# Optimization experiments

Measured on AMD Instinct MI355X. Metric: run time of the kernel, lower is better.

Reference implementation:

```python
import jax, jax.numpy as jnp
import numpy as np

B, S, D = 4, 2048, 512
H, DK = 8, 64
FFN = 2048
LEFT, CHUNK, RIGHT = 512, 128, 128
EPS = 1e-5


def _emformer_mask():
    # True = disallowed. Each query attends to its own chunk, LEFT keys before
    # the chunk start, and RIGHT keys after the chunk end.
    idx = jnp.arange(S)
    cs = (idx // CHUNK) * CHUNK                      # chunk start per query
    j = idx[None, :]
    allowed = (j >= cs[:, None] - LEFT) & (j < cs[:, None] + CHUNK + RIGHT)
    return jnp.broadcast_to(~allowed, (B, 1, S, S))


def _ln(x, g, b):
    m = jnp.mean(x, axis=-1, keepdims=True)
    v = jnp.var(x, axis=-1, keepdims=True)
    return (x - m) * jax.lax.rsqrt(v + EPS) * g + b


def setup_inputs() -> dict:
    key = jax.random.key(0)
    ks = jax.random.split(key, 8)
    w = lambda k, shp: jax.random.normal(k, shp, dtype=jnp.float32) * 0.02
    return {
        "x": jax.random.normal(ks[0], (B, S, D), dtype=jnp.float32),
        "mask": _emformer_mask(),
        "ln_in_g": jnp.ones((D,), jnp.float32), "ln_in_b": jnp.zeros((D,), jnp.float32),
        "wq": w(ks[1], (D, D)), "bq": jnp.zeros((D,), jnp.float32),
        "wk": w(ks[2], (D, D)), "bk": jnp.zeros((D,), jnp.float32),
        "wv": w(ks[3], (D, D)), "bv": jnp.zeros((D,), jnp.float32),
        "ln1_g": jnp.ones((D,), jnp.float32), "ln1_b": jnp.zeros((D,), jnp.float32),
        "w1": w(ks[4], (D, FFN)), "b1": jnp.zeros((FFN,), jnp.float32),
        "w2": w(ks[5], (FFN, D)), "b2": jnp.zeros((D,), jnp.float32),
        "ln2_g": jnp.ones((D,), jnp.float32), "ln2_b": jnp.zeros((D,), jnp.float32),
    }


def reference(x, mask, ln_in_g, ln_in_b, wq, bq, wk, bk, wv, bv,
              ln1_g, ln1_b, w1, b1, w2, b2, ln2_g, ln2_b):
    h = _ln(x, ln_in_g, ln_in_b)                                  # [B,S,D]
    q = (h @ wq + bq).reshape(B, S, H, DK).transpose(0, 2, 1, 3)   # [B,H,S,DK]
    k = (h @ wk + bk).reshape(B, S, H, DK).transpose(0, 2, 1, 3)
    v = (h @ wv + bv).reshape(B, S, H, DK).transpose(0, 2, 1, 3)
    scores = jnp.einsum("bhqd,bhkd->bhqk", q, k) / np.sqrt(DK).astype(np.float32)
    scores = jnp.where(mask, -jnp.inf, scores)
    probs = jax.nn.softmax(scores, axis=-1)
    probs = jnp.where(mask, 0.0, probs)                           # masked_fill after softmax
    out = jnp.einsum("bhqk,bhkd->bhqd", probs, v)
    out = out.transpose(0, 2, 1, 3).reshape(B, S, D)
    attn_out = out + h                                            # residual uses post-LN input
    o = _ln(attn_out, ln1_g, ln1_b)
    o = (o @ w1 + b1) @ w2 + b2 + attn_out                        # NOTE: no activation in source
    return _ln(o, ln2_g, ln2_b)
```

## Files before the change

kernel.cpp:

```cpp
#include <hip/hip_runtime.h>
#include <stdint.h>

#define B_ 4
#define S_ 2048
#define D_ 512
#define H_ 8
#define FFN_ 2048
#define M_ (B_*S_)

typedef unsigned short u16;
typedef __attribute__((ext_vector_type(8))) __bf16 bf16x8;
typedef __attribute__((ext_vector_type(8))) u16 u16x8;
typedef __attribute__((ext_vector_type(4))) u16 u16x4;
typedef __attribute__((ext_vector_type(4))) float f32x4;

__device__ __forceinline__ u16 f2bf(float f) {
  uint32_t u = __builtin_bit_cast(uint32_t, f);
  u += 0x7FFFu + ((u >> 16) & 1u);
  return (u16)(u >> 16);
}
__device__ __forceinline__ bf16x8 ldfrag(const u16* p) {
  return __builtin_bit_cast(bf16x8, *(const u16x8*)p);
}
__device__ __forceinline__ void gld16(const void* g, void* l) {
  __builtin_amdgcn_global_load_lds(
      (const __attribute__((address_space(1))) void*)g,
      (__attribute__((address_space(3))) void*)l, 16, 0, 0);
}

__global__ __launch_bounds__(256)
void wtrans(const float* __restrict__ W, int K, int N, u16* __restrict__ Wt) {
  __shared__ float t[32][33];
  int n0 = blockIdx.x * 32, k0 = blockIdx.y * 32;
  int x = threadIdx.x, y = threadIdx.y;
#pragma unroll
  for (int r = 0; r < 4; r++) t[y + 8*r][x] = W[(size_t)(k0 + y + 8*r) * N + n0 + x];
  __syncthreads();
#pragma unroll
  for (int r = 0; r < 4; r++) Wt[(size_t)(n0 + y + 8*r) * K + k0 + x] = f2bf(t[x][y + 8*r]);
}

__global__ void bcat(const float* __restrict__ bq, const float* __restrict__ bk,
                     const float* __restrict__ bv, float* __restrict__ o) {
  int i = blockIdx.x * 256 + threadIdx.x;
  o[i] = i < 512 ? bq[i] : (i < 1024 ? bk[i - 512] : bv[i - 1024]);
}

template <bool OUT32, bool OUT16, bool SUM2>
__global__ __launch_bounds__(128)
void ln_k(const float* __restrict__ x, const float* __restrict__ g,
          const float* __restrict__ bta, float* __restrict__ y32,
          u16* __restrict__ y16, const u16* __restrict__ x2) {
  int row = blockIdx.x;
  int t = threadIdx.x;
  const float* xr = x + (size_t)row * 512;
  f32x4 v = *(const f32x4*)(xr + t * 4);
  if constexpr (SUM2) {
    u16x4 p2 = *(const u16x4*)(x2 + (size_t)row * 512 + t * 4);
#pragma unroll
    for (int j = 0; j < 4; j++)
      v[j] += __builtin_bit_cast(float, (uint32_t)p2[j] << 16);
  }
  float s = v.x + v.y + v.z + v.w;
  float s2 = v.x*v.x + v.y*v.y + v.z*v.z + v.w*v.w;
#pragma unroll
  for (int m = 32; m; m >>= 1) { s += __shfl_xor(s, m); s2 += __shfl_xor(s2, m); }
  __shared__ float p[4];
  int wv = t >> 6;
  if ((t & 63) == 0) { p[wv] = s; p[2 + wv] = s2; }
  __syncthreads();
  s = p[0] + p[1]; s2 = p[2] + p[3];
  float mean = s * (1.f / 512.f);
  float var = s2 * (1.f / 512.f) - mean * mean;
  float rs = rsqrtf(var + 1e-5f);
#pragma unroll
  for (int j = 0; j < 4; j++) {
    float o = (v[j] - mean) * rs * g[t*4 + j] + bta[t*4 + j];
    if constexpr (OUT32) y32[(size_t)row * 512 + t*4 + j] = o;
    if constexpr (OUT16) y16[(size_t)row * 512 + t*4 + j] = f2bf(o);
  }
}

template <int NTW, int NCOL, int KSPLIT, bool RESID, bool OUT32, bool OUT16>
__global__ __launch_bounds__(256)
void gemm_db(const u16* __restrict__ A, const u16* __restrict__ Bt,
             const float* __restrict__ bias, int K, int N,
             const float* __restrict__ resid, float* __restrict__ C32,
             u16* __restrict__ C16) {
  __shared__ __align__(16) u16 As[2][128 * 32];
  __shared__ __align__(16) u16 Bs[2][NTW * 1024];
  const int tid = threadIdx.x;
  const int wave = tid >> 6, lane = tid & 63;
  const int l15 = lane & 15, quad = lane >> 4;
  const int wm = wave >> 1, wn = wave & 1;

  int lin = blockIdx.x;
  int kh = 0;
  if constexpr (KSPLIT == 2) {
    const int nblk = (M_ / 128) * NCOL;
    kh = lin >= nblk;
    lin -= kh * nblk;
  }
  const int rpx = (M_ / 128) / 8;
  const int xcd = lin & 7, local = lin >> 3;
  const int row0 = (xcd * rpx + local / NCOL) * 128;
  const int col0 = (local % NCOL) * (NTW * 32);
  const int klen = K / KSPLIT;
  const int kstart = kh * klen;

  f32x4 acc[4][NTW];
#pragma unroll
  for (int i = 0; i < 4; i++)
#pragma unroll
    for (int j = 0; j < NTW; j++) acc[i][j] = (f32x4){0.f, 0.f, 0.f, 0.f};

  const int lr = lane >> 2;
  const int lc = ((lane & 3) ^ ((lane >> 3) & 3)) * 8;
  const u16* aG0 = A + (size_t)(row0 + (wave * 2) * 16 + lr) * K + lc;
  const u16* aG1 = A + (size_t)(row0 + (wave * 2 + 1) * 16 + lr) * K + lc;
  const int aO0 = (wave * 2) * 512 + lane * 8;
  const int aO1 = (wave * 2 + 1) * 512 + lane * 8;
  const u16* bG[NTW / 2];
  int bO[NTW / 2];
#pragma unroll
  for (int i = 0; i < NTW / 2; i++) {
    int ch = wave * (NTW / 2) + i;
    bG[i] = Bt + (size_t)(col0 + ch * 16 + lr) * K + lc;
    bO[i] = ch * 512 + lane * 8;
  }
  const int rsw = (l15 >> 1) & 3;

  gld16(aG0 + kstart, &As[0][aO0]);
  gld16(aG1 + kstart, &As[0][aO1]);
#pragma unroll
  for (int i = 0; i < NTW / 2; i++) gld16(bG[i] + kstart, &Bs[0][bO[i]]);

  const int nIter = klen >> 5;
  for (int it = 0; it < nIter; it++) {
    __syncthreads();
    const int cur = it & 1;
    if (it + 1 < nIter) {
      const int nxt = cur ^ 1;
      const int k = kstart + ((it + 1) << 5);
      gld16(aG0 + k, &As[nxt][aO0]);
      gld16(aG1 + k, &As[nxt][aO1]);
#pragma unroll
      for (int i = 0; i < NTW / 2; i++) gld16(bG[i] + k, &Bs[nxt][bO[i]]);
    }
    bf16x8 af[4], bf[NTW];
#pragma unroll
    for (int mt = 0; mt < 4; mt++)
      af[mt] = ldfrag(&As[cur][(wm * 64 + mt * 16 + l15) * 32 + ((quad ^ rsw) * 8)]);
#pragma unroll
    for (int nt = 0; nt < NTW; nt++)
      bf[nt] = ldfrag(&Bs[cur][(wn * (NTW * 16) + nt * 16 + l15) * 32 + ((quad ^ rsw) * 8)]);
#pragma unroll
    for (int mt = 0; mt < 4; mt++)
#pragma unroll
      for (int nt = 0; nt < NTW; nt++)
        acc[mt][nt] = __builtin_amdgcn_mfma_f32_16x16x32_bf16(af[mt], bf[nt], acc[mt][nt], 0, 0, 0);
  }
#pragma unroll
  for (int mt = 0; mt < 4; mt++)
#pragma unroll
    for (int nt = 0; nt < NTW; nt++) {
      int n = col0 + wn * (NTW * 16) + nt * 16 + l15;
      float bv;
      if constexpr (KSPLIT == 2) bv = (kh == 0) ? bias[n] : 0.f;
      else bv = bias[n];
#pragma unroll
      for (int r = 0; r < 4; r++) {
        int m = row0 + wm * 64 + mt * 16 + quad * 4 + r;
        float val = acc[mt][nt][r] + bv;
        if constexpr (KSPLIT == 2) {
          if (kh == 0) C32[(size_t)m * N + n] = val + resid[(size_t)m * N + n];
          else C16[(size_t)m * N + n] = f2bf(val);
        } else {
          if constexpr (RESID) val += resid[(size_t)m * N + n];
          if constexpr (OUT32) C32[(size_t)m * N + n] = val;
          if constexpr (OUT16) C16[(size_t)m * N + n] = f2bf(val);
        }
      }
    }
}

__global__ __launch_bounds__(256)
void vtrans(const u16* __restrict__ qkv, u16* __restrict__ vt) {
  __shared__ u16 t[64][65];
  int s0 = blockIdx.x * 64, h = blockIdx.y, b = blockIdx.z;
  int x = threadIdx.x, y = threadIdx.y;
  const u16* src = qkv + (size_t)(b * 2048 + s0) * 1536 + 1024 + h * 64;
#pragma unroll
  for (int r = 0; r < 16; r++) { int s = y + 4*r; t[s][x] = src[(size_t)s * 1536 + x]; }
  __syncthreads();
  u16* dst = vt + (size_t)((b * 8 + h) * 64) * 2048 + s0;
#pragma unroll
  for (int r = 0; r < 16; r++) { int d = y + 4*r; dst[(size_t)d * 2048 + x] = t[x][d]; }
}

#define PSTR 136
__global__ __launch_bounds__(256)
void attn_k(const u16* __restrict__ qkv, const u16* __restrict__ vt,
            const float* __restrict__ hres, float* __restrict__ attn) {
  __shared__ __align__(16) u16 smem[8192 + 8192 + 64 * PSTR];
  u16* Ks = smem;
  u16* Vts = smem + 8192;
  u16* Ps = smem + 16384;
  u16* Qs = Ps;

  const int lin = blockIdx.x;
  const int xcd = lin & 7, g = lin >> 3;
  const int cq = g & 31;
  const int bh = xcd * 4 + (g >> 5);
  const int hh = bh & 7, b = bh >> 3;
  const int c = cq >> 1;
  const int s0 = cq * 64;
  const int tid = threadIdx.x, wave = tid >> 6, lane = tid & 63;
  const int l15 = lane & 15, quad = lane >> 4;
  const int t_lo = (c > 4) ? c - 4 : 0;
  const int t_hi = (c + 2 < 16) ? c + 2 : 16;
  const int l7sw = l15 & 7;

  {
    const int cg = ((lane & 7) ^ (lane >> 3)) * 8;
    const int cp = (lane & 7) * 8;
#pragma unroll
    for (int q2 = 0; q2 < 2; q2++) {
      int r = wave * 16 + q2 * 8 + (lane >> 3);
      gld16(qkv + (size_t)(b * 2048 + s0 + r) * 1536 + hh * 64 + cg, Qs + r * 64 + cp);
    }
  }
  __syncthreads();
  bf16x8 qf[2];
#pragma unroll
  for (int f = 0; f < 2; f++)
    qf[f] = ldfrag(Qs + (wave * 16 + l15) * 64 + (((f * 4 + quad) ^ l7sw) * 8));

  const u16x8 ones16 = {0x3F80, 0x3F80, 0x3F80, 0x3F80, 0x3F80, 0x3F80, 0x3F80, 0x3F80};
  const bf16x8 onesf = __builtin_bit_cast(bf16x8, ones16);

  f32x4 accO[4];
#pragma unroll
  for (int i = 0; i < 4; i++) accO[i] = (f32x4){0.f, 0.f, 0.f, 0.f};
  f32x4 accD = (f32x4){0.f, 0.f, 0.f, 0.f};

  for (int kt = t_lo; kt < t_hi; ++kt) {
    __syncthreads();
    {
      const int cgk = ((lane & 7) ^ (lane >> 3)) * 8;
      const int cpk = (lane & 7) * 8;
#pragma unroll
      for (int q2 = 0; q2 < 4; q2++) {
        int r = wave * 32 + q2 * 8 + (lane >> 3);
        gld16(qkv + (size_t)(b * 2048 + kt * 128 + r) * 1536 + 512 + hh * 64 + cgk,
              Ks + r * 64 + cpk);
      }
      const int cpv = (lane & 15) * 8;
#pragma unroll
      for (int q2 = 0; q2 < 4; q2++) {
        int d = (wave * 4 + q2) * 4 + (lane >> 4);
        int cgv = ((lane & 8) | ((lane & 7) ^ (lane >> 4) ^ ((q2 & 1) << 2))) * 8;
        gld16(vt + (size_t)((b * 8 + hh) * 64 + d) * 2048 + kt * 128 + cgv,
              Vts + d * 128 + cpv);
      }
    }
    __syncthreads();

#pragma unroll
    for (int nt = 0; nt < 8; nt++) {
      bf16x8 kf0 = ldfrag(Ks + (nt * 16 + l15) * 64 + ((quad ^ l7sw) * 8));
      bf16x8 kf1 = ldfrag(Ks + (nt * 16 + l15) * 64 + (((4 + quad) ^ l7sw) * 8));
      f32x4 s4 = (f32x4){0.f, 0.f, 0.f, 0.f};
      s4 = __builtin_amdgcn_mfma_f32_16x16x32_bf16(qf[0], kf0, s4, 0, 0, 0);
      s4 = __builtin_amdgcn_mfma_f32_16x16x32_bf16(qf[1], kf1, s4, 0, 0, 0);
#pragma unroll
      for (int r = 0; r < 4; r++) {
        float pp = exp2f(s4[r] * (1.4426950408889634f * 0.125f));
        Ps[(wave * 16 + quad * 4 + r) * PSTR + nt * 16 + l15] =
            (u16)(__builtin_bit_cast(uint32_t, pp) >> 16);
      }
    }
#pragma unroll
    for (int ki = 0; ki < 4; ki++) {
      bf16x8 pf = ldfrag(Ps + (wave * 16 + l15) * PSTR + (ki * 4 + quad) * 8);
      accD = __builtin_amdgcn_mfma_f32_16x16x32_bf16(pf, onesf, accD, 0, 0, 0);
#pragma unroll
      for (int dt = 0; dt < 4; dt++) {
        int gg = ki * 4 + quad;
        bf16x8 vf = ldfrag(Vts + (dt * 16 + l15) * 128 + (((gg & 8) | ((gg & 7) ^ l7sw)) * 8));
        accO[dt] = __builtin_amdgcn_mfma_f32_16x16x32_bf16(pf, vf, accO[dt], 0, 0, 0);
      }
    }
  }
#pragma unroll
  for (int r = 0; r < 4; r++) {
    float dinv = 1.0f / accD[r];
    int m = s0 + wave * 16 + quad * 4 + r;
#pragma unroll
    for (int dt = 0; dt < 4; dt++) {
      size_t idx = (size_t)(b * 2048 + m) * 512 + hh * 64 + dt * 16 + l15;
      attn[idx] = accO[dt][r] * dinv + hres[idx];
    }
  }
}

extern "C" void kernel_launch(void* const* d_in, const int* in_sizes, int n_in,
                              void* d_out, int out_size, void* d_ws, size_t ws_size,
                              hipStream_t stream) {
  (void)in_sizes; (void)n_in; (void)out_size; (void)ws_size;
  const float* x       = (const float*)d_in[0];
  const float* ln_in_g = (const float*)d_in[2];
  const float* ln_in_b = (const float*)d_in[3];
  const float* wq = (const float*)d_in[4];
  const float* bq = (const float*)d_in[5];
  const float* wk = (const float*)d_in[6];
  const float* bk = (const float*)d_in[7];
  const float* wv = (const float*)d_in[8];
  const float* bv = (const float*)d_in[9];
  const float* ln1_g = (const float*)d_in[10];
  const float* ln1_b = (const float*)d_in[11];
  const float* w1 = (const float*)d_in[12];
  const float* b1 = (const float*)d_in[13];
  const float* w2 = (const float*)d_in[14];
  const float* b2 = (const float*)d_in[15];
  const float* ln2_g = (const float*)d_in[16];
  const float* ln2_b = (const float*)d_in[17];

  char* ws = (char*)d_ws;
  size_t off = 0;
  auto alloc = [&](size_t bytes) {
    void* p = ws + off;
    off = (off + bytes + 255) & ~(size_t)255;
    return p;
  };
  u16*   wqkvt = (u16*)  alloc((size_t)1536 * 512 * 2);
  float* bqkv  = (float*)alloc(1536 * 4);
  u16*   w1t   = (u16*)  alloc((size_t)2048 * 512 * 2);
  u16*   w2t   = (u16*)  alloc((size_t)512 * 2048 * 2);
  float* h32   = (float*)alloc((size_t)M_ * 512 * 4);
  u16*   h16   = (u16*)  alloc((size_t)M_ * 512 * 2);
  u16*   qkv16 = (u16*)  alloc((size_t)M_ * 1536 * 2);
  u16*   vtb   = (u16*)  alloc((size_t)B_ * H_ * 64 * 2048 * 2);
  float* attn32= (float*)alloc((size_t)M_ * 512 * 4);
  float* out2  = h32;
  u16*   o16   = h16;
  u16*   f16b  = qkv16;

  wtrans<<<dim3(16, 16), dim3(32, 8), 0, stream>>>(wq, 512, 512, wqkvt);
  wtrans<<<dim3(16, 16), dim3(32, 8), 0, stream>>>(wk, 512, 512, wqkvt + (size_t)512 * 512);
  wtrans<<<dim3(16, 16), dim3(32, 8), 0, stream>>>(wv, 512, 512, wqkvt + (size_t)1024 * 512);
  wtrans<<<dim3(64, 16), dim3(32, 8), 0, stream>>>(w1, 512, 2048, w1t);
  wtrans<<<dim3(16, 64), dim3(32, 8), 0, stream>>>(w2, 2048, 512, w2t);
  bcat<<<6, 256, 0, stream>>>(bq, bk, bv, bqkv);

  ln_k<true, true, false><<<M_, 128, 0, stream>>>(x, ln_in_g, ln_in_b, h32, h16, nullptr);
  gemm_db<4, 12, 1, false, false, true><<<dim3(12 * 64), 256, 0, stream>>>(
      h16, wqkvt, bqkv, 512, 1536, nullptr, nullptr, qkv16);
  vtrans<<<dim3(32, 8, 4), dim3(64, 4), 0, stream>>>(qkv16, vtb);
  attn_k<<<dim3(1024), 256, 0, stream>>>(qkv16, vtb, h32, attn32);
  ln_k<false, true, false><<<M_, 128, 0, stream>>>(attn32, ln1_g, ln1_b, nullptr, o16, nullptr);
  gemm_db<4, 16, 1, false, false, true><<<dim3(16 * 64), 256, 0, stream>>>(
      o16, w1t, b1, 512, 2048, nullptr, nullptr, f16b);
  gemm_db<2, 8, 2, false, false, false><<<dim3(2 * 8 * 64), 256, 0, stream>>>(
      f16b, w2t, b2, 2048, 512, attn32, out2, h16);
  ln_k<true, false, true><<<M_, 128, 0, stream>>>(out2, ln2_g, ln2_b, (float*)d_out, nullptr, h16);
}
```

Baseline: 296.2 us.

## Triple-buffer GEMM loads, double-buffer attention K/V, swizzle P, merge QKV transposes

The GEMM main loop moves from double to triple buffering. It now uses explicit vmcnt waits plus s_barrier instead of a full __syncthreads, so two tiles of global loads stay in flight. The attention kernel double-buffers its K/V tiles and prefetches the next tile while computing the current one. The padded P buffer is replaced with an XOR-swizzled layout. The three Q/K/V weight-transpose launches are merged into one, and the FFN1 GEMM switches to narrower column tiles (NTW 2, 32 column blocks). Together these aim to hide load latency and cut launch overhead, at the cost of more LDS per block (lower occupancy) and fragile hand-counted vmcnt values.

```diff
diff --git a/kernel.cpp b/kernel.cpp
--- a/kernel.cpp
+++ b/kernel.cpp
@@ -27,6 +27,16 @@
       (const __attribute__((address_space(1))) void*)g,
       (__attribute__((address_space(3))) void*)l, 16, 0, 0);
 }
+template <int N>
+__device__ __forceinline__ void wait_vm_barrier() {
+  if constexpr (N == 0)      asm volatile("s_waitcnt vmcnt(0)\n\ts_barrier" ::: "memory");
+  else if constexpr (N == 3) asm volatile("s_waitcnt vmcnt(3)\n\ts_barrier" ::: "memory");
+  else if constexpr (N == 4) asm volatile("s_waitcnt vmcnt(4)\n\ts_barrier" ::: "memory");
+  else if constexpr (N == 8) asm volatile("s_waitcnt vmcnt(8)\n\ts_barrier" ::: "memory");
+}
+__device__ __forceinline__ void barrier_only() {
+  asm volatile("s_barrier" ::: "memory");
+}
 
 __global__ __launch_bounds__(256)
 void wtrans(const float* __restrict__ W, int K, int N, u16* __restrict__ Wt) {
@@ -38,6 +48,22 @@
   __syncthreads();
 #pragma unroll
   for (int r = 0; r < 4; r++) Wt[(size_t)(n0 + y + 8*r) * K + k0 + x] = f2bf(t[x][y + 8*r]);
+}
+
+__global__ __launch_bounds__(256)
+void wtrans3(const float* __restrict__ Wq, const float* __restrict__ Wk,
+             const float* __restrict__ Wv, u16* __restrict__ Wt) {
+  __shared__ float t[32][33];
+  int z = blockIdx.z;
+  const float* W = z == 0 ? Wq : (z == 1 ? Wk : Wv);
+  u16* dst = Wt + (size_t)z * 512 * 512;
+  int n0 = blockIdx.x * 32, k0 = blockIdx.y * 32;
+  int x = threadIdx.x, y = threadIdx.y;
+#pragma unroll
+  for (int r = 0; r < 4; r++) t[y + 8*r][x] = W[(size_t)(k0 + y + 8*r) * 512 + n0 + x];
+  __syncthreads();
+#pragma unroll
+  for (int r = 0; r < 4; r++) dst[(size_t)(n0 + y + 8*r) * 512 + k0 + x] = f2bf(t[x][y + 8*r]);
 }
 
 __global__ void bcat(const float* __restrict__ bq, const float* __restrict__ bk,
@@ -87,8 +113,8 @@
              const float* __restrict__ bias, int K, int N,
              const float* __restrict__ resid, float* __restrict__ C32,
              u16* __restrict__ C16) {
-  __shared__ __align__(16) u16 As[2][128 * 32];
-  __shared__ __align__(16) u16 Bs[2][NTW * 1024];
+  __shared__ __align__(16) u16 As[3][128 * 32];
+  __shared__ __align__(16) u16 Bs[3][NTW * 1024];
   const int tid = threadIdx.x;
   const int wave = tid >> 6, lane = tid & 63;
   const int l15 = lane & 15, quad = lane >> 4;
@@ -129,24 +155,25 @@
     bO[i] = ch * 512 + lane * 8;
   }
   const int rsw = (l15 >> 1) & 3;
-
-  gld16(aG0 + kstart, &As[0][aO0]);
-  gld16(aG1 + kstart, &As[0][aO1]);
-#pragma unroll
-  for (int i = 0; i < NTW / 2; i++) gld16(bG[i] + kstart, &Bs[0][bO[i]]);
+  constexpr int L = 2 + NTW / 2;
+
+  auto issue = [&](int kof, int buf) {
+    gld16(aG0 + kof, &As[buf][aO0]);
+    gld16(aG1 + kof, &As[buf][aO1]);
+#pragma unroll
+    for (int i = 0; i < NTW / 2; i++) gld16(bG[i] + kof, &Bs[buf][bO[i]]);
+  };
 
   const int nIter = klen >> 5;
+  issue(kstart, 0);
+  issue(kstart + 32, 1);
+
+  int cur = 0;
   for (int it = 0; it < nIter; it++) {
-    __syncthreads();
-    const int cur = it & 1;
-    if (it + 1 < nIter) {
-      const int nxt = cur ^ 1;
-      const int k = kstart + ((it + 1) << 5);
-      gld16(aG0 + k, &As[nxt][aO0]);
-      gld16(aG1 + k, &As[nxt][aO1]);
-#pragma unroll
-      for (int i = 0; i < NTW / 2; i++) gld16(bG[i] + k, &Bs[nxt][bO[i]]);
-    }
+    if (it + 1 < nIter) wait_vm_barrier<L>();
+    else wait_vm_barrier<0>();
+    int pf = cur + 2; if (pf >= 3) pf -= 3;
+    if (it + 2 < nIter) issue(kstart + ((it + 2) << 5), pf);
     bf16x8 af[4], bf[NTW];
 #pragma unroll
     for (int mt = 0; mt < 4; mt++)
@@ -159,6 +186,7 @@
 #pragma unroll
       for (int nt = 0; nt < NTW; nt++)
         acc[mt][nt] = __builtin_amdgcn_mfma_f32_16x16x32_bf16(af[mt], bf[nt], acc[mt][nt], 0, 0, 0);
+    cur = cur == 2 ? 0 : cur + 1;
   }
 #pragma unroll
   for (int mt = 0; mt < 4; mt++)
@@ -198,14 +226,13 @@
   for (int r = 0; r < 16; r++) { int d = y + 4*r; dst[(size_t)d * 2048 + x] = t[x][d]; }
 }
 
-#define PSTR 136
 __global__ __launch_bounds__(256)
 void attn_k(const u16* __restrict__ qkv, const u16* __restrict__ vt,
             const float* __restrict__ hres, float* __restrict__ attn) {
-  __shared__ __align__(16) u16 smem[8192 + 8192 + 64 * PSTR];
+  __shared__ __align__(16) u16 smem[2 * 8192 + 2 * 8192 + 64 * 128];
   u16* Ks = smem;
-  u16* Vts = smem + 8192;
-  u16* Ps = smem + 16384;
+  u16* Vts = smem + 16384;
+  u16* Ps = smem + 32768;
   u16* Qs = Ps;
 
   const int lin = blockIdx.x;
@@ -221,15 +248,34 @@
   const int t_hi = (c + 2 < 16) ? c + 2 : 16;
   const int l7sw = l15 & 7;
 
+  const int cgk = ((lane & 7) ^ (lane >> 3)) * 8;
+  const int cpk = (lane & 7) * 8;
+  const int cpv = (lane & 15) * 8;
+
+  auto issueKV = [&](int kt, int buf) {
+#pragma unroll
+    for (int q2 = 0; q2 < 4; q2++) {
+      int r = wave * 32 + q2 * 8 + (lane >> 3);
+      gld16(qkv + (size_t)(b * 2048 + kt * 128 + r) * 1536 + 512 + hh * 64 + cgk,
+            Ks + buf * 8192 + r * 64 + cpk);
+    }
+#pragma unroll
+    for (int q2 = 0; q2 < 4; q2++) {
+      int d = (wave * 4 + q2) * 4 + (lane >> 4);
+      int cgv = ((lane & 8) | ((lane & 7) ^ (lane >> 4) ^ ((q2 & 1) << 2))) * 8;
+      gld16(vt + (size_t)((b * 8 + hh) * 64 + d) * 2048 + kt * 128 + cgv,
+            Vts + buf * 8192 + d * 128 + cpv);
+    }
+  };
+
   {
-    const int cg = ((lane & 7) ^ (lane >> 3)) * 8;
-    const int cp = (lane & 7) * 8;
 #pragma unroll
     for (int q2 = 0; q2 < 2; q2++) {
       int r = wave * 16 + q2 * 8 + (lane >> 3);
-      gld16(qkv + (size_t)(b * 2048 + s0 + r) * 1536 + hh * 64 + cg, Qs + r * 64 + cp);
-    }
-  }
+      gld16(qkv + (size_t)(b * 2048 + s0 + r) * 1536 + hh * 64 + cgk, Qs + r * 64 + cpk);
+    }
+  }
+  issueKV(t_lo, 0);
   __syncthreads();
   bf16x8 qf[2];
 #pragma unroll
@@ -245,49 +291,40 @@
   f32x4 accD = (f32x4){0.f, 0.f, 0.f, 0.f};
 
   for (int kt = t_lo; kt < t_hi; ++kt) {
-    __syncthreads();
-    {
-      const int cgk = ((lane & 7) ^ (lane >> 3)) * 8;
-      const int cpk = (lane & 7) * 8;
-#pragma unroll
-      for (int q2 = 0; q2 < 4; q2++) {
-        int r = wave * 32 + q2 * 8 + (lane >> 3);
-        gld16(qkv + (size_t)(b * 2048 + kt * 128 + r) * 1536 + 512 + hh * 64 + cgk,
-              Ks + r * 64 + cpk);
-      }
-      const int cpv = (lane & 15) * 8;
-#pragma unroll
-      for (int q2 = 0; q2 < 4; q2++) {
-        int d = (wave * 4 + q2) * 4 + (lane >> 4);
-        int cgv = ((lane & 8) | ((lane & 7) ^ (lane >> 4) ^ ((q2 & 1) << 2))) * 8;
-        gld16(vt + (size_t)((b * 8 + hh) * 64 + d) * 2048 + kt * 128 + cgv,
-              Vts + d * 128 + cpv);
-      }
-    }
-    __syncthreads();
+    const int j = kt - t_lo, cur = j & 1, nxt = cur ^ 1;
+    barrier_only();
+    if (kt + 1 < t_hi) {
+      issueKV(kt + 1, nxt);
+      wait_vm_barrier<8>();
+    } else {
+      wait_vm_barrier<0>();
+    }
+    const u16* Kc = Ks + cur * 8192;
+    const u16* Vc = Vts + cur * 8192;
 
 #pragma unroll
     for (int nt = 0; nt < 8; nt++) {
-      bf16x8 kf0 = ldfrag(Ks + (nt * 16 + l15) * 64 + ((quad ^ l7sw) * 8));
-      bf16x8 kf1 = ldfrag(Ks + (nt * 16 + l15) * 64 + (((4 + quad) ^ l7sw) * 8));
+      bf16x8 kf0 = ldfrag(Kc + (nt * 16 + l15) * 64 + ((quad ^ l7sw) * 8));
+      bf16x8 kf1 = ldfrag(Kc + (nt * 16 + l15) * 64 + (((4 + quad) ^ l7sw) * 8));
       f32x4 s4 = (f32x4){0.f, 0.f, 0.f, 0.f};
       s4 = __builtin_amdgcn_mfma_f32_16x16x32_bf16(qf[0], kf0, s4, 0, 0, 0);
       s4 = __builtin_amdgcn_mfma_f32_16x16x32_bf16(qf[1], kf1, s4, 0, 0, 0);
 #pragma unroll
       for (int r = 0; r < 4; r++) {
         float pp = exp2f(s4[r] * (1.4426950408889634f * 0.125f));
-        Ps[(wave * 16 + quad * 4 + r) * PSTR + nt * 16 + l15] =
+        Ps[(wave * 16 + quad * 4 + r) * 128 +
+           (((nt * 2 + (l15 >> 3)) ^ (quad * 4 + r)) * 8) + (l15 & 7)] =
             (u16)(__builtin_bit_cast(uint32_t, pp) >> 16);
       }
     }
 #pragma unroll
     for (int ki = 0; ki < 4; ki++) {
-      bf16x8 pf = ldfrag(Ps + (wave * 16 + l15) * PSTR + (ki * 4 + quad) * 8);
+      bf16x8 pf = ldfrag(Ps + (wave * 16 + l15) * 128 + (((ki * 4 + quad) ^ l15) * 8));
       accD = __builtin_amdgcn_mfma_f32_16x16x32_bf16(pf, onesf, accD, 0, 0, 0);
 #pragma unroll
       for (int dt = 0; dt < 4; dt++) {
         int gg = ki * 4 + quad;
-        bf16x8 vf = ldfrag(Vts + (dt * 16 + l15) * 128 + (((gg & 8) | ((gg & 7) ^ l7sw)) * 8));
+        bf16x8 vf = ldfrag(Vc + (dt * 16 + l15) * 128 + (((gg & 8) | ((gg & 7) ^ l7sw)) * 8));
         accO[dt] = __builtin_amdgcn_mfma_f32_16x16x32_bf16(pf, vf, accO[dt], 0, 0, 0);
       }
     }
@@ -346,9 +383,7 @@
   u16*   o16   = h16;
   u16*   f16b  = qkv16;
 
-  wtrans<<<dim3(16, 16), dim3(32, 8), 0, stream>>>(wq, 512, 512, wqkvt);
-  wtrans<<<dim3(16, 16), dim3(32, 8), 0, stream>>>(wk, 512, 512, wqkvt + (size_t)512 * 512);
-  wtrans<<<dim3(16, 16), dim3(32, 8), 0, stream>>>(wv, 512, 512, wqkvt + (size_t)1024 * 512);
+  wtrans3<<<dim3(16, 16, 3), dim3(32, 8), 0, stream>>>(wq, wk, wv, wqkvt);
   wtrans<<<dim3(64, 16), dim3(32, 8), 0, stream>>>(w1, 512, 2048, w1t);
   wtrans<<<dim3(16, 64), dim3(32, 8), 0, stream>>>(w2, 2048, 512, w2t);
   bcat<<<6, 256, 0, stream>>>(bq, bk, bv, bqkv);
@@ -359,7 +394,7 @@
   vtrans<<<dim3(32, 8, 4), dim3(64, 4), 0, stream>>>(qkv16, vtb);
   attn_k<<<dim3(1024), 256, 0, stream>>>(qkv16, vtb, h32, attn32);
   ln_k<false, true, false><<<M_, 128, 0, stream>>>(attn32, ln1_g, ln1_b, nullptr, o16, nullptr);
-  gemm_db<4, 16, 1, false, false, true><<<dim3(16 * 64), 256, 0, stream>>>(
+  gemm_db<2, 32, 1, false, false, true><<<dim3(32 * 64), 256, 0, stream>>>(
       o16, w1t, b1, 512, 2048, nullptr, nullptr, f16b);
   gemm_db<2, 8, 2, false, false, false><<<dim3(2 * 8 * 64), 256, 0, stream>>>(
       f16b, w2t, b2, 2048, 512, attn32, out2, h16);
```

New measurement: 293.5 us. No clear change (-0.9%).

## Triple-buffer GEMM loads, merge weight prep kernels, widen attention and GEMM tiles

Applied to the files above, without the earlier changes.

The GEMM main loop moves from double to triple buffering. It uses explicit vmcnt waits plus barriers so two k-tiles are in flight at once. The six weight-transpose and bias-concat launches become one prep kernel. The attention kernel now handles 128 queries per block, two 64-row groups sharing K/V loads, and the FFN GEMMs use wider N tiles. Together these aim to cut load latency stalls, launch overhead and redundant K/V traffic, at the cost of more LDS, more registers and fewer blocks.

```diff
diff --git a/kernel.cpp b/kernel.cpp
--- a/kernel.cpp
+++ b/kernel.cpp
@@ -27,23 +27,48 @@
       (const __attribute__((address_space(1))) void*)g,
       (__attribute__((address_space(3))) void*)l, 16, 0, 0);
 }
+template <int N>
+__device__ __forceinline__ void wait_vm_barrier() {
+  if constexpr (N == 0)      asm volatile("s_waitcnt vmcnt(0)\n\ts_barrier" ::: "memory");
+  else if constexpr (N == 3) asm volatile("s_waitcnt vmcnt(3)\n\ts_barrier" ::: "memory");
+  else if constexpr (N == 4) asm volatile("s_waitcnt vmcnt(4)\n\ts_barrier" ::: "memory");
+  else if constexpr (N == 6) asm volatile("s_waitcnt vmcnt(6)\n\ts_barrier" ::: "memory");
+  else if constexpr (N == 8) asm volatile("s_waitcnt vmcnt(8)\n\ts_barrier" ::: "memory");
+}
 
 __global__ __launch_bounds__(256)
-void wtrans(const float* __restrict__ W, int K, int N, u16* __restrict__ Wt) {
+void prep(const float* __restrict__ wq, const float* __restrict__ wk,
+          const float* __restrict__ wv, const float* __restrict__ w1,
+          const float* __restrict__ w2, const float* __restrict__ bq,
+          const float* __restrict__ bk, const float* __restrict__ bv,
+          u16* __restrict__ wqkvt, u16* __restrict__ w1t,
+          u16* __restrict__ w2t, float* __restrict__ bqkv) {
+  int id = blockIdx.x, tid = threadIdx.x;
+  if (id >= 2816) {
+    int i = (id - 2816) * 256 + tid;
+    bqkv[i] = i < 512 ? bq[i] : (i < 1024 ? bk[i - 512] : bv[i - 1024]);
+    return;
+  }
   __shared__ float t[32][33];
-  int n0 = blockIdx.x * 32, k0 = blockIdx.y * 32;
-  int x = threadIdx.x, y = threadIdx.y;
+  const float* W; u16* dst; int K, N, bx, by;
+  if (id < 768) {
+    int z = id >> 8, r = id & 255;
+    W = z == 0 ? wq : (z == 1 ? wk : wv);
+    dst = wqkvt + (size_t)z * 512 * 512; K = 512; N = 512;
+    bx = r & 15; by = r >> 4;
+  } else if (id < 1792) {
+    int r = id - 768; W = w1; dst = w1t; K = 512; N = 2048;
+    bx = r & 63; by = r >> 6;
+  } else {
+    int r = id - 1792; W = w2; dst = w2t; K = 2048; N = 512;
+    bx = r & 15; by = r >> 4;
+  }
+  int n0 = bx * 32, k0 = by * 32, x = tid & 31, y = tid >> 5;
 #pragma unroll
   for (int r = 0; r < 4; r++) t[y + 8*r][x] = W[(size_t)(k0 + y + 8*r) * N + n0 + x];
   __syncthreads();
 #pragma unroll
-  for (int r = 0; r < 4; r++) Wt[(size_t)(n0 + y + 8*r) * K + k0 + x] = f2bf(t[x][y + 8*r]);
-}
-
-__global__ void bcat(const float* __restrict__ bq, const float* __restrict__ bk,
-                     const float* __restrict__ bv, float* __restrict__ o) {
-  int i = blockIdx.x * 256 + threadIdx.x;
-  o[i] = i < 512 ? bq[i] : (i < 1024 ? bk[i - 512] : bv[i - 1024]);
+  for (int r = 0; r < 4; r++) dst[(size_t)(n0 + y + 8*r) * K + k0 + x] = f2bf(t[x][y + 8*r]);
 }
 
 template <bool OUT32, bool OUT16, bool SUM2>
@@ -87,8 +112,8 @@
              const float* __restrict__ bias, int K, int N,
              const float* __restrict__ resid, float* __restrict__ C32,
              u16* __restrict__ C16) {
-  __shared__ __align__(16) u16 As[2][128 * 32];
-  __shared__ __align__(16) u16 Bs[2][NTW * 1024];
+  __shared__ __align__(16) u16 As[3][128 * 32];
+  __shared__ __align__(16) u16 Bs[3][NTW * 1024];
   const int tid = threadIdx.x;
   const int wave = tid >> 6, lane = tid & 63;
   const int l15 = lane & 15, quad = lane >> 4;
@@ -129,24 +154,25 @@
     bO[i] = ch * 512 + lane * 8;
   }
   const int rsw = (l15 >> 1) & 3;
-
-  gld16(aG0 + kstart, &As[0][aO0]);
-  gld16(aG1 + kstart, &As[0][aO1]);
-#pragma unroll
-  for (int i = 0; i < NTW / 2; i++) gld16(bG[i] + kstart, &Bs[0][bO[i]]);
+  constexpr int L = 2 + NTW / 2;
+
+  auto issue = [&](int kof, int buf) {
+    gld16(aG0 + kof, &As[buf][aO0]);
+    gld16(aG1 + kof, &As[buf][aO1]);
+#pragma unroll
+    for (int i = 0; i < NTW / 2; i++) gld16(bG[i] + kof, &Bs[buf][bO[i]]);
+  };
 
   const int nIter = klen >> 5;
+  issue(kstart, 0);
+  issue(kstart + 32, 1);
+
+  int cur = 0;
   for (int it = 0; it < nIter; it++) {
-    __syncthreads();
-    const int cur = it & 1;
-    if (it + 1 < nIter) {
-      const int nxt = cur ^ 1;
-      const int k = kstart + ((it + 1) << 5);
-      gld16(aG0 + k, &As[nxt][aO0]);
-      gld16(aG1 + k, &As[nxt][aO1]);
-#pragma unroll
-      for (int i = 0; i < NTW / 2; i++) gld16(bG[i] + k, &Bs[nxt][bO[i]]);
-    }
+    if (it + 1 < nIter) wait_vm_barrier<L>();
+    else wait_vm_barrier<0>();
+    int pf = cur + 2; if (pf >= 3) pf -= 3;
+    if (it + 2 < nIter) issue(kstart + ((it + 2) << 5), pf);
     bf16x8 af[4], bf[NTW];
 #pragma unroll
     for (int mt = 0; mt < 4; mt++)
@@ -159,6 +185,7 @@
 #pragma unroll
       for (int nt = 0; nt < NTW; nt++)
         acc[mt][nt] = __builtin_amdgcn_mfma_f32_16x16x32_bf16(af[mt], bf[nt], acc[mt][nt], 0, 0, 0);
+    cur = cur == 2 ? 0 : cur + 1;
   }
 #pragma unroll
   for (int mt = 0; mt < 4; mt++)
@@ -202,7 +229,7 @@
 __global__ __launch_bounds__(256)
 void attn_k(const u16* __restrict__ qkv, const u16* __restrict__ vt,
             const float* __restrict__ hres, float* __restrict__ attn) {
-  __shared__ __align__(16) u16 smem[8192 + 8192 + 64 * PSTR];
+  __shared__ __align__(16) u16 smem[8192 + 8192 + 128 * PSTR];
   u16* Ks = smem;
   u16* Vts = smem + 8192;
   u16* Ps = smem + 16384;
@@ -210,11 +237,10 @@
 
   const int lin = blockIdx.x;
   const int xcd = lin & 7, g = lin >> 3;
-  const int cq = g & 31;
-  const int bh = xcd * 4 + (g >> 5);
+  const int c = g & 15;
+  const int bh = xcd * 4 + (g >> 4);
   const int hh = bh & 7, b = bh >> 3;
-  const int c = cq >> 1;
-  const int s0 = cq * 64;
+  const int s0 = c * 128;
   const int tid = threadIdx.x, wave = tid >> 6, lane = tid & 63;
   const int l15 = lane & 15, quad = lane >> 4;
   const int t_lo = (c > 4) ? c - 4 : 0;
@@ -225,24 +251,28 @@
     const int cg = ((lane & 7) ^ (lane >> 3)) * 8;
     const int cp = (lane & 7) * 8;
 #pragma unroll
-    for (int q2 = 0; q2 < 2; q2++) {
-      int r = wave * 16 + q2 * 8 + (lane >> 3);
+    for (int q2 = 0; q2 < 4; q2++) {
+      int r = wave * 32 + q2 * 8 + (lane >> 3);
       gld16(qkv + (size_t)(b * 2048 + s0 + r) * 1536 + hh * 64 + cg, Qs + r * 64 + cp);
     }
   }
   __syncthreads();
-  bf16x8 qf[2];
-#pragma unroll
-  for (int f = 0; f < 2; f++)
-    qf[f] = ldfrag(Qs + (wave * 16 + l15) * 64 + (((f * 4 + quad) ^ l7sw) * 8));
+  bf16x8 qf[2][2];
+#pragma unroll
+  for (int qg = 0; qg < 2; qg++)
+#pragma unroll
+    for (int f = 0; f < 2; f++)
+      qf[qg][f] = ldfrag(Qs + (qg * 64 + wave * 16 + l15) * 64 + (((f * 4 + quad) ^ l7sw) * 8));
 
   const u16x8 ones16 = {0x3F80, 0x3F80, 0x3F80, 0x3F80, 0x3F80, 0x3F80, 0x3F80, 0x3F80};
   const bf16x8 onesf = __builtin_bit_cast(bf16x8, ones16);
 
-  f32x4 accO[4];
-#pragma unroll
-  for (int i = 0; i < 4; i++) accO[i] = (f32x4){0.f, 0.f, 0.f, 0.f};
-  f32x4 accD = (f32x4){0.f, 0.f, 0.f, 0.f};
+  f32x4 accO[2][4];
+#pragma unroll
+  for (int qg = 0; qg < 2; qg++)
+#pragma unroll
+    for (int i = 0; i < 4; i++) accO[qg][i] = (f32x4){0.f, 0.f, 0.f, 0.f};
+  f32x4 accD[2] = {(f32x4){0.f, 0.f, 0.f, 0.f}, (f32x4){0.f, 0.f, 0.f, 0.f}};
 
   for (int kt = t_lo; kt < t_hi; ++kt) {
     __syncthreads();
@@ -270,38 +300,49 @@
     for (int nt = 0; nt < 8; nt++) {
       bf16x8 kf0 = ldfrag(Ks + (nt * 16 + l15) * 64 + ((quad ^ l7sw) * 8));
       bf16x8 kf1 = ldfrag(Ks + (nt * 16 + l15) * 64 + (((4 + quad) ^ l7sw) * 8));
-      f32x4 s4 = (f32x4){0.f, 0.f, 0.f, 0.f};
-      s4 = __builtin_amdgcn_mfma_f32_16x16x32_bf16(qf[0], kf0, s4, 0, 0, 0);
-      s4 = __builtin_amdgcn_mfma_f32_16x16x32_bf16(qf[1], kf1, s4, 0, 0, 0);
-#pragma unroll
-      for (int r = 0; r < 4; r++) {
-        float pp = exp2f(s4[r] * (1.4426950408889634f * 0.125f));
-        Ps[(wave * 16 + quad * 4 + r) * PSTR + nt * 16 + l15] =
-            (u16)(__builtin_bit_cast(uint32_t, pp) >> 16);
+#pragma unroll
+      for (int qg = 0; qg < 2; qg++) {
+        f32x4 s4 = (f32x4){0.f, 0.f, 0.f, 0.f};
+        s4 = __builtin_amdgcn_mfma_f32_16x16x32_bf16(qf[qg][0], kf0, s4, 0, 0, 0);
+        s4 = __builtin_amdgcn_mfma_f32_16x16x32_bf16(qf[qg][1], kf1, s4, 0, 0, 0);
+#pragma unroll
+        for (int r = 0; r < 4; r++) {
+          float pp = exp2f(s4[r] * (1.4426950408889634f * 0.125f));
+          Ps[(qg * 64 + wave * 16 + quad * 4 + r) * PSTR + nt * 16 + l15] =
+              (u16)(__builtin_bit_cast(uint32_t, pp) >> 16);
+        }
       }
     }
 #pragma unroll
     for (int ki = 0; ki < 4; ki++) {
-      bf16x8 pf = ldfrag(Ps + (wave * 16 + l15) * PSTR + (ki * 4 + quad) * 8);
-      accD = __builtin_amdgcn_mfma_f32_16x16x32_bf16(pf, onesf, accD, 0, 0, 0);
+      bf16x8 pf[2];
+#pragma unroll
+      for (int qg = 0; qg < 2; qg++) {
+        pf[qg] = ldfrag(Ps + (qg * 64 + wave * 16 + l15) * PSTR + (ki * 4 + quad) * 8);
+        accD[qg] = __builtin_amdgcn_mfma_f32_16x16x32_bf16(pf[qg], onesf, accD[qg], 0, 0, 0);
+      }
 #pragma unroll
       for (int dt = 0; dt < 4; dt++) {
         int gg = ki * 4 + quad;
         bf16x8 vf = ldfrag(Vts + (dt * 16 + l15) * 128 + (((gg & 8) | ((gg & 7) ^ l7sw)) * 8));
-        accO[dt] = __builtin_amdgcn_mfma_f32_16x16x32_bf16(pf, vf, accO[dt], 0, 0, 0);
-      }
-    }
-  }
-#pragma unroll
-  for (int r = 0; r < 4; r++) {
-    float dinv = 1.0f / accD[r];
-    int m = s0 + wave * 16 + quad * 4 + r;
-#pragma unroll
-    for (int dt = 0; dt < 4; dt++) {
-      size_t idx = (size_t)(b * 2048 + m) * 512 + hh * 64 + dt * 16 + l15;
-      attn[idx] = accO[dt][r] * dinv + hres[idx];
-    }
-  }
+#pragma unroll
+        for (int qg = 0; qg < 2; qg++)
+          accO[qg][dt] = __builtin_amdgcn_mfma_f32_16x16x32_bf16(pf[qg], vf, accO[qg][dt], 0, 0, 0);
+      }
+    }
+  }
+#pragma unroll
+  for (int qg = 0; qg < 2; qg++)
+#pragma unroll
+    for (int r = 0; r < 4; r++) {
+      float dinv = 1.0f / accD[qg][r];
+      int m = s0 + qg * 64 + wave * 16 + quad * 4 + r;
+#pragma unroll
+      for (int dt = 0; dt < 4; dt++) {
+        size_t idx = (size_t)(b * 2048 + m) * 512 + hh * 64 + dt * 16 + l15;
+        attn[idx] = accO[qg][dt][r] * dinv + hres[idx];
+      }
+    }
 }
 
 extern "C" void kernel_launch(void* const* d_in, const int* in_sizes, int n_in,
@@ -346,22 +387,18 @@
   u16*   o16   = h16;
   u16*   f16b  = qkv16;
 
-  wtrans<<<dim3(16, 16), dim3(32, 8), 0, stream>>>(wq, 512, 512, wqkvt);
-  wtrans<<<dim3(16, 16), dim3(32, 8), 0, stream>>>(wk, 512, 512, wqkvt + (size_t)512 * 512);
-  wtrans<<<dim3(16, 16), dim3(32, 8), 0, stream>>>(wv, 512, 512, wqkvt + (size_t)1024 * 512);
-  wtrans<<<dim3(64, 16), dim3(32, 8), 0, stream>>>(w1, 512, 2048, w1t);
-  wtrans<<<dim3(16, 64), dim3(32, 8), 0, stream>>>(w2, 2048, 512, w2t);
-  bcat<<<6, 256, 0, stream>>>(bq, bk, bv, bqkv);
+  prep<<<dim3(2822), 256, 0, stream>>>(wq, wk, wv, w1, w2, bq, bk, bv,
+                                       wqkvt, w1t, w2t, bqkv);
 
   ln_k<true, true, false><<<M_, 128, 0, stream>>>(x, ln_in_g, ln_in_b, h32, h16, nullptr);
   gemm_db<4, 12, 1, false, false, true><<<dim3(12 * 64), 256, 0, stream>>>(
       h16, wqkvt, bqkv, 512, 1536, nullptr, nullptr, qkv16);
   vtrans<<<dim3(32, 8, 4), dim3(64, 4), 0, stream>>>(qkv16, vtb);
-  attn_k<<<dim3(1024), 256, 0, stream>>>(qkv16, vtb, h32, attn32);
+  attn_k<<<dim3(512), 256, 0, stream>>>(qkv16, vtb, h32, attn32);
   ln_k<false, true, false><<<M_, 128, 0, stream>>>(attn32, ln1_g, ln1_b, nullptr, o16, nullptr);
-  gemm_db<4, 16, 1, false, false, true><<<dim3(16 * 64), 256, 0, stream>>>(
+  gemm_db<8, 8, 1, false, false, true><<<dim3(8 * 64), 256, 0, stream>>>(
       o16, w1t, b1, 512, 2048, nullptr, nullptr, f16b);
-  gemm_db<2, 8, 2, false, false, false><<<dim3(2 * 8 * 64), 256, 0, stream>>>(
+  gemm_db<4, 4, 2, false, false, false><<<dim3(2 * 4 * 64), 256, 0, stream>>>(
       f16b, w2t, b2, 2048, 512, attn32, out2, h16);
   ln_k<true, false, true><<<M_, 128, 0, stream>>>(out2, ln2_g, ln2_b, (float*)d_out, nullptr, h16);
 }
```

After: 299.8 us. No clear change (+1.2%).
